# Kernel optimization log

Measured on AMD Instinct MI355X. Metric: run time of the kernel, lower is better.

The kernel has to match this reference:

```python
import jax, jax.numpy as jnp
from jax import lax
import numpy as np

KPAD = 2  # padding for 5x5 kernel, 'same' output

def setup_inputs() -> dict:
    key = jax.random.key(0)
    x = jax.random.normal(key, (16, 8, 512, 512), dtype=jnp.float32)
    # fixed 5x5 averaging kernel, matching torch.ones(5,5)/25
    weight = jnp.ones((1, 1, 5, 5), dtype=jnp.float32) / 25.0
    return {"x": x, "weight": weight}

def reference(x, weight):
    # Per-channel (depthwise) 5x5 box blur. The torch code loops conv2d over
    # split channels; a single grouped conv with feature_group_count=C is the
    # same math in one fused op.
    C = x.shape[1]
    k = jnp.tile(weight, (C, 1, 1, 1))  # (C,1,5,5) OIHW with groups=C
    return lax.conv_general_dilated(
        x, k,
        window_strides=(1, 1),
        padding=[(KPAD, KPAD), (KPAD, KPAD)],
        dimension_numbers=("NCHW", "OIHW", "NCHW"),
        feature_group_count=C,
    )
```

## Files before the change

### kernel.cpp

```cpp
#include <hip/hip_runtime.h>


#define H 512
#define W 512
#define RB 32
#define GR 16

struct RowV { float2 l; float4 m; float2 r; };

__device__ __forceinline__ RowV load_row(const float* __restrict__ in, int rr,
                                         int offL, int c0, int offR) {
    const int rc = rr < 0 ? 0 : (rr > (H - 1) ? (H - 1) : rr);
    const float* p = in + (size_t)rc * W;
    RowV v;
    v.l = *reinterpret_cast<const float2*>(p + offL);
    v.m = *reinterpret_cast<const float4*>(p + c0);
    v.r = *reinterpret_cast<const float2*>(p + offR);
    return v;
}

__device__ __forceinline__ void hsum4(const RowV& v, float mrow, float mL, float mR,
                                      float& s0, float& s1, float& s2, float& s3) {
    const float a0 = v.l.x * mL, a1 = v.l.y * mL;
    const float b4 = v.r.x * mR, b5 = v.r.y * mR;
    const float t1 = v.m.x + v.m.y;
    const float t2 = v.m.z + v.m.w;
    s0 = (a0 + a1 + t1 + v.m.z) * mrow;
    s1 = (a1 + t1 + t2) * mrow;
    s2 = (t1 + t2 + b4) * mrow;
    s3 = (v.m.y + t2 + b4 + b5) * mrow;
}

__global__ __launch_bounds__(256) void avefilter_kernel(
    const float* __restrict__ x, const float* __restrict__ wgt,
    float* __restrict__ out)
{
    const int t     = threadIdx.x;
    const int g     = t >> 7;
    const int lt    = t & 127;
    const int c0    = lt << 2;
    const int plane = blockIdx.y;
    const int r0    = blockIdx.x * RB + g * GR;

    const float* in = x + (size_t)plane * (H * W);
    float* op = out + (size_t)plane * (H * W) + (size_t)r0 * W + c0;
    const float scale = wgt[0];

    const float mL = (lt != 0)   ? 1.f : 0.f;
    const float mR = (lt != 127) ? 1.f : 0.f;
    const int  offL = (lt != 0)   ? (c0 - 2) : c0;
    const int  offR = (lt != 127) ? (c0 + 4) : c0;

    float h[4][5];

    RowV p0  = load_row(in, r0 - 2, offL, c0, offR);
    RowV p1  = load_row(in, r0 - 1, offL, c0, offR);
    RowV p2  = load_row(in, r0,     offL, c0, offR);
    RowV p3  = load_row(in, r0 + 1, offL, c0, offR);
    RowV cur = load_row(in, r0 + 2, offL, c0, offR);

    const float mtop = (r0 == 0) ? 0.f : 1.f;
    hsum4(p0, mtop, mL, mR, h[0][0], h[1][0], h[2][0], h[3][0]);
    hsum4(p1, mtop, mL, mR, h[0][1], h[1][1], h[2][1], h[3][1]);
    hsum4(p2, 1.f,  mL, mR, h[0][2], h[1][2], h[2][2], h[3][2]);
    hsum4(p3, 1.f,  mL, mR, h[0][3], h[1][3], h[2][3], h[3][3]);

    #pragma unroll
    for (int i = 0; i < GR - 1; ++i) {
        RowV nxt = load_row(in, r0 + 3 + i, offL, c0, offR);
        const int   s    = (i + 4) % 5;
        const float mrow = ((unsigned)(r0 + 2 + i) < (unsigned)H) ? 1.f : 0.f;
        hsum4(cur, mrow, mL, mR, h[0][s], h[1][s], h[2][s], h[3][s]);
        float4 o;
        o.x = (h[0][0] + h[0][1] + h[0][2] + h[0][3] + h[0][4]) * scale;
        o.y = (h[1][0] + h[1][1] + h[1][2] + h[1][3] + h[1][4]) * scale;
        o.z = (h[2][0] + h[2][1] + h[2][2] + h[2][3] + h[2][4]) * scale;
        o.w = (h[3][0] + h[3][1] + h[3][2] + h[3][3] + h[3][4]) * scale;
        *reinterpret_cast<float4*>(op + (size_t)i * W) = o;
        cur = nxt;
    }
    {
        const int   i    = GR - 1;
        const int   s    = (i + 4) % 5;
        const float mrow = ((unsigned)(r0 + 2 + i) < (unsigned)H) ? 1.f : 0.f;
        hsum4(cur, mrow, mL, mR, h[0][s], h[1][s], h[2][s], h[3][s]);
        float4 o;
        o.x = (h[0][0] + h[0][1] + h[0][2] + h[0][3] + h[0][4]) * scale;
        o.y = (h[1][0] + h[1][1] + h[1][2] + h[1][3] + h[1][4]) * scale;
        o.z = (h[2][0] + h[2][1] + h[2][2] + h[2][3] + h[2][4]) * scale;
        o.w = (h[3][0] + h[3][1] + h[3][2] + h[3][3] + h[3][4]) * scale;
        *reinterpret_cast<float4*>(op + (size_t)i * W) = o;
    }
}

extern "C" void kernel_launch(void* const* d_in, const int* in_sizes, int n_in,
                              void* d_out, int out_size, void* d_ws, size_t ws_size,
                              hipStream_t stream) {
    const float* x   = (const float*)d_in[0];
    const float* wgt = (const float*)d_in[1];
    float* out = (float*)d_out;

    dim3 grid(H / RB, 16 * 8);
    dim3 block(256);
    avefilter_kernel<<<grid, block, 0, stream>>>(x, wgt, out);
}
```

Baseline: 231.7 us.

## Software-pipeline row loads with inline asm and explicit vmcnt waits

Replaces compiler-generated row loads with inline-asm global_load instructions held in a 5-deep ring buffer. Explicit s_waitcnt vmcnt counts and sched barriers keep four rows of loads in flight while the current row is processed. This aims to hide global memory latency better than the compiler's scheduling did. The cost is that correctness now depends on hand-counted vmcnt values, which could break if the compiler inserts other vector memory ops (stores also count against vmcnt on some targets).

```diff
diff --git a/kernel.cpp b/kernel.cpp
--- a/kernel.cpp
+++ b/kernel.cpp
@@ -4,22 +4,27 @@
 #define H 512
 #define W 512
 #define RB 32
-#define GR 16
 
-struct RowV { float2 l; float4 m; float2 r; };
+typedef float f32x4 __attribute__((ext_vector_type(4)));
+typedef float f32x2 __attribute__((ext_vector_type(2)));
 
-__device__ __forceinline__ RowV load_row(const float* __restrict__ in, int rr,
-                                         int offL, int c0, int offR) {
+struct RowB { f32x2 l; f32x4 m; f32x2 r; };
+
+__device__ __forceinline__ void issue_row(RowB& b, const float* __restrict__ in,
+                                          int rr, int offL, int c0, int offR) {
     const int rc = rr < 0 ? 0 : (rr > (H - 1) ? (H - 1) : rr);
     const float* p = in + (size_t)rc * W;
-    RowV v;
-    v.l = *reinterpret_cast<const float2*>(p + offL);
-    v.m = *reinterpret_cast<const float4*>(p + c0);
-    v.r = *reinterpret_cast<const float2*>(p + offR);
-    return v;
+    asm volatile("global_load_dwordx2 %0, %1, off" : "=&v"(b.l) : "v"(p + offL));
+    asm volatile("global_load_dwordx4 %0, %1, off" : "=&v"(b.m) : "v"(p + c0));
+    asm volatile("global_load_dwordx2 %0, %1, off" : "=&v"(b.r) : "v"(p + offR));
 }
 
-__device__ __forceinline__ void hsum4(const RowV& v, float mrow, float mL, float mR,
+#define WAITVM(N) do {                                            \
+    asm volatile("s_waitcnt vmcnt(" #N ")" ::: "memory");         \
+    __builtin_amdgcn_sched_barrier(0);                            \
+} while (0)
+
+__device__ __forceinline__ void hsum4(const RowB& v, float mrow, float mL, float mR,
                                       float& s0, float& s1, float& s2, float& s3) {
     const float a0 = v.l.x * mL, a1 = v.l.y * mL;
     const float b4 = v.r.x * mR, b5 = v.r.y * mR;
@@ -40,7 +45,7 @@
     const int lt    = t & 127;
     const int c0    = lt << 2;
     const int plane = blockIdx.y;
-    const int r0    = blockIdx.x * RB + g * GR;
+    const int r0    = blockIdx.x * RB + g * 16;
 
     const float* in = x + (size_t)plane * (H * W);
     float* op = out + (size_t)plane * (H * W) + (size_t)r0 * W + c0;
@@ -51,45 +56,38 @@
     const int  offL = (lt != 0)   ? (c0 - 2) : c0;
     const int  offR = (lt != 127) ? (c0 + 4) : c0;
 
+    RowB buf[5];
     float h[4][5];
 
-    RowV p0  = load_row(in, r0 - 2, offL, c0, offR);
-    RowV p1  = load_row(in, r0 - 1, offL, c0, offR);
-    RowV p2  = load_row(in, r0,     offL, c0, offR);
-    RowV p3  = load_row(in, r0 + 1, offL, c0, offR);
-    RowV cur = load_row(in, r0 + 2, offL, c0, offR);
-
-    const float mtop = (r0 == 0) ? 0.f : 1.f;
-    hsum4(p0, mtop, mL, mR, h[0][0], h[1][0], h[2][0], h[3][0]);
-    hsum4(p1, mtop, mL, mR, h[0][1], h[1][1], h[2][1], h[3][1]);
-    hsum4(p2, 1.f,  mL, mR, h[0][2], h[1][2], h[2][2], h[3][2]);
-    hsum4(p3, 1.f,  mL, mR, h[0][3], h[1][3], h[2][3], h[3][3]);
+    issue_row(buf[0], in, r0 - 2, offL, c0, offR);
+    issue_row(buf[1], in, r0 - 1, offL, c0, offR);
+    issue_row(buf[2], in, r0,     offL, c0, offR);
+    issue_row(buf[3], in, r0 + 1, offL, c0, offR);
 
     #pragma unroll
-    for (int i = 0; i < GR - 1; ++i) {
-        RowV nxt = load_row(in, r0 + 3 + i, offL, c0, offR);
-        const int   s    = (i + 4) % 5;
-        const float mrow = ((unsigned)(r0 + 2 + i) < (unsigned)H) ? 1.f : 0.f;
-        hsum4(cur, mrow, mL, mR, h[0][s], h[1][s], h[2][s], h[3][s]);
-        float4 o;
-        o.x = (h[0][0] + h[0][1] + h[0][2] + h[0][3] + h[0][4]) * scale;
-        o.y = (h[1][0] + h[1][1] + h[1][2] + h[1][3] + h[1][4]) * scale;
-        o.z = (h[2][0] + h[2][1] + h[2][2] + h[2][3] + h[2][4]) * scale;
-        o.w = (h[3][0] + h[3][1] + h[3][2] + h[3][3] + h[3][4]) * scale;
-        *reinterpret_cast<float4*>(op + (size_t)i * W) = o;
-        cur = nxt;
-    }
-    {
-        const int   i    = GR - 1;
-        const int   s    = (i + 4) % 5;
-        const float mrow = ((unsigned)(r0 + 2 + i) < (unsigned)H) ? 1.f : 0.f;
-        hsum4(cur, mrow, mL, mR, h[0][s], h[1][s], h[2][s], h[3][s]);
-        float4 o;
-        o.x = (h[0][0] + h[0][1] + h[0][2] + h[0][3] + h[0][4]) * scale;
-        o.y = (h[1][0] + h[1][1] + h[1][2] + h[1][3] + h[1][4]) * scale;
-        o.z = (h[2][0] + h[2][1] + h[2][2] + h[2][3] + h[2][4]) * scale;
-        o.w = (h[3][0] + h[3][1] + h[3][2] + h[3][3] + h[3][4]) * scale;
-        *reinterpret_cast<float4*>(op + (size_t)i * W) = o;
+    for (int i = 0; i < 20; ++i) {
+        if (i + 4 < 20)
+            issue_row(buf[(i + 4) % 5], in, r0 + 2 + i, offL, c0, offR);
+
+        if      (i <= 15) WAITVM(12);
+        else if (i == 16) WAITVM(9);
+        else if (i == 17) WAITVM(6);
+        else if (i == 18) WAITVM(3);
+        else              WAITVM(0);
+
+        const int   rr   = r0 - 2 + i;
+        const float mrow = ((unsigned)rr < (unsigned)H) ? 1.f : 0.f;
+        const int   s    = i % 5;
+        hsum4(buf[s], mrow, mL, mR, h[0][s], h[1][s], h[2][s], h[3][s]);
+
+        if (i >= 4) {
+            float4 o;
+            o.x = (h[0][0] + h[0][1] + h[0][2] + h[0][3] + h[0][4]) * scale;
+            o.y = (h[1][0] + h[1][1] + h[1][2] + h[1][3] + h[1][4]) * scale;
+            o.z = (h[2][0] + h[2][1] + h[2][2] + h[2][3] + h[2][4]) * scale;
+            o.w = (h[3][0] + h[3][1] + h[3][2] + h[3][3] + h[3][4]) * scale;
+            *reinterpret_cast<float4*>(op + (size_t)(i - 4) * W) = o;
+        }
     }
 }
 
```

New measurement: 227.6 us. Within noise of the previous version (-1.8%).
